# Kernel tuning notes

Measured on AMD Instinct MI355X. Metric: run time of the kernel, lower is better.

The kernel has to match this reference:

```python
import jax, jax.numpy as jnp
import numpy as np

NUM_HEADS = 16
LN_EPS = 1e-05


def setup_inputs() -> dict:
    key = jax.random.key(0)
    ks = jax.random.split(key, 10)
    B, S, H = 2, 2048, 1024
    s = 1.0 / np.sqrt(H)
    return {
        "hidden_states": jax.random.normal(ks[0], (B, S, H), dtype=jnp.float32),
        "Wq": jax.random.normal(ks[1], (H, H), dtype=jnp.float32) * s,
        "bq": jax.random.normal(ks[2], (H,), dtype=jnp.float32) * 0.02,
        "Wk": jax.random.normal(ks[3], (H, H), dtype=jnp.float32) * s,
        "bk": jax.random.normal(ks[4], (H,), dtype=jnp.float32) * 0.02,
        "Wv": jax.random.normal(ks[5], (H, H), dtype=jnp.float32) * s,
        "bv": jax.random.normal(ks[6], (H,), dtype=jnp.float32) * 0.02,
        "Wd": jax.random.normal(ks[7], (H, H), dtype=jnp.float32) * s,
        "bd": jax.random.normal(ks[8], (H,), dtype=jnp.float32) * 0.02,
        "ln_gamma": jnp.ones((H,), dtype=jnp.float32),
        "ln_beta": jnp.zeros((H,), dtype=jnp.float32),
    }


def reference(hidden_states, Wq, bq, Wk, bk, Wv, bv, Wd, bd, ln_gamma, ln_beta):
    B, S, H = hidden_states.shape
    nh = NUM_HEADS
    hd = H // nh

    # QKV projections (torch Linear: x @ W.T + b), split heads -> [B, nh, S, hd]
    def proj(W, b):
        y = jnp.einsum('bsh,oh->bso', hidden_states, W) + b
        return y.reshape(B, S, nh, hd).transpose(0, 2, 1, 3)

    q = proj(Wq, bq)
    k = proj(Wk, bk)
    v = proj(Wv, bv)

    # scaled dot-product attention: [B, nh, S, S]
    scores = jnp.einsum('bhqd,bhkd->bhqk', q, k) / jnp.sqrt(jnp.float32(hd))
    probs = jax.nn.softmax(scores, axis=-1)
    ctx = jnp.einsum('bhqk,bhkd->bhqd', probs, v)  # [B, nh, S, hd]
    ctx = ctx.transpose(0, 2, 1, 3).reshape(B, S, H)

    # output dense + residual + LayerNorm
    attn_out = jnp.einsum('bsh,oh->bso', ctx, Wd) + bd
    x = attn_out + hidden_states
    mu = jnp.mean(x, axis=-1, keepdims=True)
    var = jnp.mean(jnp.square(x - mu), axis=-1, keepdims=True)
    return (x - mu) * jax.lax.rsqrt(var + LN_EPS) * ln_gamma + ln_beta
```

## Files before the change

kernel.cpp:

```cpp
#include <hip/hip_runtime.h>

constexpr int kH    = 1024;
constexpr int kSEQ  = 2048;
constexpr int kBATCH= 2;
constexpr int kNH   = 16;
constexpr int kHD   = 64;
constexpr int kM    = 4096;

typedef _Float16 h8  __attribute__((ext_vector_type(8)));
typedef _Float16 h4  __attribute__((ext_vector_type(4)));
typedef float   f32x4 __attribute__((ext_vector_type(4)));

static __device__ __forceinline__ f32x4 mfma16(h8 a, h8 b, f32x4 c) {
  return __builtin_amdgcn_mfma_f32_16x16x32_f16(a, b, c, 0, 0, 0);
}

static __device__ __forceinline__ void gll16(const _Float16* g, _Float16* l) {
  __builtin_amdgcn_global_load_lds(
      (const __attribute__((address_space(1))) void*)g,
      (__attribute__((address_space(3))) void*)l, 16, 0, 0);
}

#define QSCALE 0.18033688011112042f
#define C0INIT (-5.770780163555854f)

__global__ __launch_bounds__(256) void cvt_all(
    const float* __restrict__ X,  const float* __restrict__ Wq,
    const float* __restrict__ Wk, const float* __restrict__ Wv,
    const float* __restrict__ Wd,
    _Float16* __restrict__ Xh,  _Float16* __restrict__ Wqh,
    _Float16* __restrict__ Wkh, _Float16* __restrict__ Wvh,
    _Float16* __restrict__ Wdh)
{
  int i = blockIdx.x * 256 + threadIdx.x;
  const float* src; _Float16* dst; int off;
  if (i < (kM * kH) / 4) {
    src = X; dst = Xh; off = i;
  } else {
    int j = i - (kM * kH) / 4;
    int w = j >> 18;
    off = j & 262143;
    src = (w == 0) ? Wq : (w == 1) ? Wk : (w == 2) ? Wv : Wd;
    dst = (w == 0) ? Wqh : (w == 1) ? Wkh : (w == 2) ? Wvh : Wdh;
  }
  float4 v = reinterpret_cast<const float4*>(src)[off];
  h4 o;
  o[0] = (_Float16)v.x; o[1] = (_Float16)v.y;
  o[2] = (_Float16)v.z; o[3] = (_Float16)v.w;
  reinterpret_cast<h4*>(dst)[off] = o;
}

__global__ __launch_bounds__(256, 2) void qkv_gemm(
    const _Float16* __restrict__ Xh,
    const _Float16* __restrict__ Wq, const _Float16* __restrict__ Wk,
    const _Float16* __restrict__ Wv,
    const float* __restrict__ bq, const float* __restrict__ bk,
    const float* __restrict__ bv,
    _Float16* __restrict__ Qo, _Float16* __restrict__ Ko, _Float16* __restrict__ Vo)
{
  const int proj = blockIdx.z;
  const _Float16* W   = (proj == 0) ? Wq : ((proj == 1) ? Wk : Wv);
  const float*    bias= (proj == 0) ? bq : ((proj == 1) ? bk : bv);
  _Float16*       Out = (proj == 0) ? Qo : ((proj == 1) ? Ko : Vo);

  const int m0 = blockIdx.y * 128, n0 = blockIdx.x * 128;
  __shared__ __align__(16) _Float16 As[2][128 * 32];
  __shared__ __align__(16) _Float16 Bs[2][128 * 32];

  const int tid  = threadIdx.x;
  const int wave = tid >> 6, lane = tid & 63, quad = lane >> 4, l16 = lane & 15;
  const int mw = (wave & 1) * 64, nw = (wave >> 1) * 64;

  f32x4 acc[4][4] = {};
  const int grow = wave * 32 + (lane >> 2);
  const int gcol = (lane & 3) * 8;
  const _Float16* Ag = Xh + (size_t)(m0 + grow) * kH + gcol;
  const _Float16* Bg = W  + (size_t)(n0 + grow) * kH + gcol;

  {
    gll16(Ag,            &As[0][wave * 1024]);
    gll16(Ag + 16 * kH,  &As[0][wave * 1024 + 512]);
    gll16(Bg,            &Bs[0][wave * 1024]);
    gll16(Bg + 16 * kH,  &Bs[0][wave * 1024 + 512]);
  }

  for (int k = 0; k < 32; ++k) {
    const int cur = k & 1;
    __syncthreads();
    if (k < 31) {
      const int k0 = (k + 1) * 32, nb = cur ^ 1;
      gll16(Ag + k0,           &As[nb][wave * 1024]);
      gll16(Ag + 16 * kH + k0, &As[nb][wave * 1024 + 512]);
      gll16(Bg + k0,           &Bs[nb][wave * 1024]);
      gll16(Bg + 16 * kH + k0, &Bs[nb][wave * 1024 + 512]);
    }
    h8 af[4], bf[4];
    #pragma unroll
    for (int mi = 0; mi < 4; ++mi)
      af[mi] = *reinterpret_cast<const h8*>(&As[cur][(mw + mi * 16 + l16) * 32 + quad * 8]);
    #pragma unroll
    for (int ni = 0; ni < 4; ++ni)
      bf[ni] = *reinterpret_cast<const h8*>(&Bs[cur][(nw + ni * 16 + l16) * 32 + quad * 8]);
    #pragma unroll
    for (int mi = 0; mi < 4; ++mi)
      #pragma unroll
      for (int ni = 0; ni < 4; ++ni)
        acc[mi][ni] = mfma16(af[mi], bf[ni], acc[mi][ni]);
  }

  #pragma unroll
  for (int mi = 0; mi < 4; ++mi)
  #pragma unroll
  for (int ni = 0; ni < 4; ++ni) {
    const int ng = n0 + nw + ni * 16 + l16;
    const float bv_ = bias[ng];
    const int hh = ng >> 6, dd = ng & 63;
    #pragma unroll
    for (int r = 0; r < 4; ++r) {
      const int mg = m0 + mw + mi * 16 + quad * 4 + r;
      float val = acc[mi][ni][r] + bv_;
      if (proj == 0) val *= QSCALE;
      const int bb = mg >> 11, srow = mg & 2047;
      Out[(((size_t)(bb * kNH + hh) * kSEQ) + srow) * kHD + dd] = (_Float16)val;
    }
  }
}

__global__ __launch_bounds__(256) void vtrans(const _Float16* __restrict__ V,
                                              _Float16* __restrict__ Vt)
{
  const int st = blockIdx.x;
  const int bh = blockIdx.y;
  __shared__ __align__(16) _Float16 Lt[64][72];
  const int t = threadIdx.x, r = t >> 2, c = (t & 3) * 16;
  const _Float16* src = V + (size_t)bh * kSEQ * kHD + (size_t)(st * 64 + r) * kHD + c;
  h8 p0 = *reinterpret_cast<const h8*>(src);
  h8 p1 = *reinterpret_cast<const h8*>(src + 8);
  #pragma unroll
  for (int e = 0; e < 8; ++e) Lt[c + e][r] = p0[e];
  #pragma unroll
  for (int e = 0; e < 8; ++e) Lt[c + 8 + e][r] = p1[e];
  __syncthreads();
  _Float16* dst = Vt + (size_t)bh * kHD * kSEQ + (size_t)r * kSEQ + st * 64 + c;
  *reinterpret_cast<h8*>(dst)     = *reinterpret_cast<const h8*>(&Lt[r][c]);
  *reinterpret_cast<h8*>(dst + 8) = *reinterpret_cast<const h8*>(&Lt[r][c + 8]);
}

__global__ __launch_bounds__(256, 3) void attn_kernel(
    const _Float16* __restrict__ Q, const _Float16* __restrict__ K,
    const _Float16* __restrict__ Vt, _Float16* __restrict__ Ctx)
{
  const int qt = blockIdx.x, bh = blockIdx.y;
  const int tid = threadIdx.x;
  const int wave = tid >> 6, lane = tid & 63, quad = lane >> 4, l16 = lane & 15;
  const int sw = l16 & 7;

  __shared__ __align__(16) _Float16 Kl[2][64 * 64];
  __shared__ __align__(16) _Float16 Vl[2][64 * 64];
  __shared__ __align__(16) _Float16 Pl[4][32 * 64];

  const _Float16* Qb = Q  + (size_t)bh * kSEQ * kHD;
  const _Float16* Kb = K  + (size_t)bh * kSEQ * kHD;
  const _Float16* Vb = Vt + (size_t)bh * kHD * kSEQ;

  const int qbase = qt * 128 + wave * 32;
  h8 qf[2][2];
  #pragma unroll
  for (int qh = 0; qh < 2; ++qh)
    #pragma unroll
    for (int dh = 0; dh < 2; ++dh)
      qf[qh][dh] = *reinterpret_cast<const h8*>(
          &Qb[(size_t)(qbase + qh * 16 + l16) * kHD + dh * 32 + quad * 8]);

  const int srow0  = lane >> 3;
  const int schunk = (lane & 7) ^ srow0;
  const int krow   = wave * 16 + srow0;
  const _Float16* Kg = Kb + (size_t)krow * kHD + schunk * 8;
  const _Float16* Vg = Vb + (size_t)krow * kSEQ + schunk * 8;
  _Float16* PlW = Pl[wave];

  float l_acc0 = 0.f, l_acc1 = 0.f;
  f32x4 o[2][4] = {};

  {
    gll16(Kg,                 &Kl[0][(wave * 16) * 64]);
    gll16(Kg + 8 * kHD,       &Kl[0][(wave * 16 + 8) * 64]);
    gll16(Vg,                 &Vl[0][(wave * 16) * 64]);
    gll16(Vg + 8 * kSEQ,      &Vl[0][(wave * 16 + 8) * 64]);
  }

  for (int kt = 0; kt < kSEQ / 64; ++kt) {
    const int cur = kt & 1;
    __syncthreads();
    if (kt + 1 < kSEQ / 64) {
      const int nb = cur ^ 1;
      const size_t ko = (size_t)(kt + 1) * 64;
      gll16(Kg + ko * kHD,             &Kl[nb][(wave * 16) * 64]);
      gll16(Kg + (ko + 8) * kHD,       &Kl[nb][(wave * 16 + 8) * 64]);
      gll16(Vg + ko,                   &Vl[nb][(wave * 16) * 64]);
      gll16(Vg + 8 * kSEQ + ko,        &Vl[nb][(wave * 16 + 8) * 64]);
    }
    const _Float16* Kc = Kl[cur];
    const _Float16* Vc = Vl[cur];

    f32x4 s[4][2];
    #pragma unroll
    for (int nt = 0; nt < 4; ++nt) {
      const int keyl = nt * 16 + l16;
      h8 ka0 = *reinterpret_cast<const h8*>(&Kc[keyl * 64 + ((quad     ) ^ sw) * 8]);
      h8 ka1 = *reinterpret_cast<const h8*>(&Kc[keyl * 64 + ((quad ^ 4) ^ sw) * 8]);
      #pragma unroll
      for (int qh = 0; qh < 2; ++qh) {
        f32x4 a = {C0INIT, C0INIT, C0INIT, C0INIT};
        a = mfma16(ka0, qf[qh][0], a);
        a = mfma16(ka1, qf[qh][1], a);
        s[nt][qh] = a;
      }
    }
    #pragma unroll
    for (int nt = 0; nt < 4; ++nt)
      #pragma unroll
      for (int qh = 0; qh < 2; ++qh) {
        float e0 = exp2f(s[nt][qh][0]);
        float e1 = exp2f(s[nt][qh][1]);
        float e2 = exp2f(s[nt][qh][2]);
        float e3 = exp2f(s[nt][qh][3]);
        float t4 = (e0 + e1) + (e2 + e3);
        if (qh == 0) l_acc0 += t4; else l_acc1 += t4;
        h4 pp;
        pp[0] = (_Float16)e0; pp[1] = (_Float16)e1;
        pp[2] = (_Float16)e2; pp[3] = (_Float16)e3;
        const int c8 = (nt * 2 + (quad >> 1)) ^ sw;
        *reinterpret_cast<h4*>(&PlW[(qh * 16 + l16) * 64 + c8 * 8 + (quad & 1) * 4]) = pp;
      }
    #pragma unroll
    for (int kc = 0; kc < 2; ++kc) {
      const int cs = ((kc * 4 + quad) ^ sw) * 8;
      h8 pa0 = *reinterpret_cast<const h8*>(&PlW[l16 * 64 + cs]);
      h8 pa1 = *reinterpret_cast<const h8*>(&PlW[(16 + l16) * 64 + cs]);
      #pragma unroll
      for (int dt = 0; dt < 4; ++dt) {
        h8 vbf = *reinterpret_cast<const h8*>(&Vc[(dt * 16 + l16) * 64 + cs]);
        o[0][dt] = mfma16(pa0, vbf, o[0][dt]);
        o[1][dt] = mfma16(pa1, vbf, o[1][dt]);
      }
    }
  }

  float li[2] = {l_acc0, l_acc1};
  #pragma unroll
  for (int qh = 0; qh < 2; ++qh) {
    li[qh] += __shfl_xor(li[qh], 16);
    li[qh] += __shfl_xor(li[qh], 32);
    li[qh] = 1.f / li[qh];
  }
  const int b = bh >> 4, hh = bh & 15;
  #pragma unroll
  for (int qh = 0; qh < 2; ++qh)
    #pragma unroll
    for (int r = 0; r < 4; ++r) {
      const float linv = __shfl(li[qh], quad * 4 + r);
      const int srow = qbase + qh * 16 + quad * 4 + r;
      #pragma unroll
      for (int dt = 0; dt < 4; ++dt) {
        const int col = hh * kHD + dt * 16 + l16;
        Ctx[((size_t)(b * kSEQ + srow)) * kH + col] =
            (_Float16)(o[qh][dt][r] * linv);
      }
    }
}

__global__ __launch_bounds__(256, 2) void dense_gemm(
    const _Float16* __restrict__ A, const _Float16* __restrict__ W,
    const float* __restrict__ bias, const float* __restrict__ resid,
    float* __restrict__ Out)
{
  const int m0 = blockIdx.y * 128, n0 = blockIdx.x * 128;
  __shared__ __align__(16) _Float16 As[2][128 * 32];
  __shared__ __align__(16) _Float16 Bs[2][128 * 32];
  const int tid  = threadIdx.x;
  const int wave = tid >> 6, lane = tid & 63, quad = lane >> 4, l16 = lane & 15;
  const int mw = (wave & 1) * 64, nw = (wave >> 1) * 64;
  f32x4 acc[4][4] = {};
  const int grow = wave * 32 + (lane >> 2);
  const int gcol = (lane & 3) * 8;
  const _Float16* Ag = A + (size_t)(m0 + grow) * kH + gcol;
  const _Float16* Bg = W + (size_t)(n0 + grow) * kH + gcol;

  {
    gll16(Ag,           &As[0][wave * 1024]);
    gll16(Ag + 16 * kH, &As[0][wave * 1024 + 512]);
    gll16(Bg,           &Bs[0][wave * 1024]);
    gll16(Bg + 16 * kH, &Bs[0][wave * 1024 + 512]);
  }

  for (int k = 0; k < 32; ++k) {
    const int cur = k & 1;
    __syncthreads();
    if (k < 31) {
      const int k0 = (k + 1) * 32, nb = cur ^ 1;
      gll16(Ag + k0,           &As[nb][wave * 1024]);
      gll16(Ag + 16 * kH + k0, &As[nb][wave * 1024 + 512]);
      gll16(Bg + k0,           &Bs[nb][wave * 1024]);
      gll16(Bg + 16 * kH + k0, &Bs[nb][wave * 1024 + 512]);
    }
    h8 af[4], bf[4];
    #pragma unroll
    for (int mi = 0; mi < 4; ++mi)
      af[mi] = *reinterpret_cast<const h8*>(&As[cur][(mw + mi * 16 + l16) * 32 + quad * 8]);
    #pragma unroll
    for (int ni = 0; ni < 4; ++ni)
      bf[ni] = *reinterpret_cast<const h8*>(&Bs[cur][(nw + ni * 16 + l16) * 32 + quad * 8]);
    #pragma unroll
    for (int mi = 0; mi < 4; ++mi)
      #pragma unroll
      for (int ni = 0; ni < 4; ++ni)
        acc[mi][ni] = mfma16(af[mi], bf[ni], acc[mi][ni]);
  }
  #pragma unroll
  for (int mi = 0; mi < 4; ++mi)
  #pragma unroll
  for (int ni = 0; ni < 4; ++ni) {
    const int ng = n0 + nw + ni * 16 + l16;
    const float bv_ = bias[ng];
    #pragma unroll
    for (int r = 0; r < 4; ++r) {
      const int mg = m0 + mw + mi * 16 + quad * 4 + r;
      Out[(size_t)mg * kH + ng] = acc[mi][ni][r] + bv_ + resid[(size_t)mg * kH + ng];
    }
  }
}

__global__ __launch_bounds__(256) void ln_kernel(const float* __restrict__ Tmp,
    const float* __restrict__ gamma, const float* __restrict__ beta,
    float* __restrict__ out)
{
  const int row = blockIdx.x;
  const float4 v = reinterpret_cast<const float4*>(Tmp + (size_t)row * kH)[threadIdx.x];
  float s  = v.x + v.y + v.z + v.w;
  float ss = v.x * v.x + v.y * v.y + v.z * v.z + v.w * v.w;
  #pragma unroll
  for (int off = 32; off > 0; off >>= 1) {
    s  += __shfl_down(s, off);
    ss += __shfl_down(ss, off);
  }
  __shared__ float red[8];
  const int wave = threadIdx.x >> 6, lane = threadIdx.x & 63;
  if (lane == 0) { red[wave] = s; red[4 + wave] = ss; }
  __syncthreads();
  s  = red[0] + red[1] + red[2] + red[3];
  ss = red[4] + red[5] + red[6] + red[7];
  const float mu   = s * (1.f / kH);
  const float var  = ss * (1.f / kH) - mu * mu;
  const float rstd = rsqrtf(var + 1e-5f);
  const float4 g  = reinterpret_cast<const float4*>(gamma)[threadIdx.x];
  const float4 bb = reinterpret_cast<const float4*>(beta)[threadIdx.x];
  float4 o;
  o.x = (v.x - mu) * rstd * g.x + bb.x;
  o.y = (v.y - mu) * rstd * g.y + bb.y;
  o.z = (v.z - mu) * rstd * g.z + bb.z;
  o.w = (v.w - mu) * rstd * g.w + bb.w;
  reinterpret_cast<float4*>(out + (size_t)row * kH)[threadIdx.x] = o;
}

extern "C" void kernel_launch(void* const* d_in, const int* in_sizes, int n_in,
                              void* d_out, int out_size, void* d_ws, size_t ws_size,
                              hipStream_t stream) {
  const float* hs    = (const float*)d_in[0];
  const float* Wq    = (const float*)d_in[1];
  const float* bq    = (const float*)d_in[2];
  const float* Wk    = (const float*)d_in[3];
  const float* bk    = (const float*)d_in[4];
  const float* Wv    = (const float*)d_in[5];
  const float* bv    = (const float*)d_in[6];
  const float* Wd    = (const float*)d_in[7];
  const float* bd    = (const float*)d_in[8];
  const float* gamma = (const float*)d_in[9];
  const float* beta  = (const float*)d_in[10];
  float* out = (float*)d_out;

  char* ws = (char*)d_ws;
  _Float16* Xh  = (_Float16*)(ws + 0);
  _Float16* Wqh = (_Float16*)(ws + 8388608);
  _Float16* Wkh = (_Float16*)(ws + 10485760);
  _Float16* Wvh = (_Float16*)(ws + 12582912);
  _Float16* Wdh = (_Float16*)(ws + 14680064);
  _Float16* Qh  = (_Float16*)(ws + 16777216);
  _Float16* Kh  = (_Float16*)(ws + 25165824);
  _Float16* Vh  = (_Float16*)(ws + 33554432);
  _Float16* Ch  = (_Float16*)(ws + 41943040);
  _Float16* Vtb = Xh;
  float*    Tmp = (float*)Qh;

  cvt_all<<<8192, 256, 0, stream>>>(hs, Wq, Wk, Wv, Wd, Xh, Wqh, Wkh, Wvh, Wdh);
  qkv_gemm<<<dim3(kH / 128, kM / 128, 3), 256, 0, stream>>>(
      Xh, Wqh, Wkh, Wvh, bq, bk, bv, Qh, Kh, Vh);
  vtrans<<<dim3(kSEQ / 64, kBATCH * kNH), 256, 0, stream>>>(Vh, Vtb);
  attn_kernel<<<dim3(kSEQ / 128, kBATCH * kNH), 256, 0, stream>>>(Qh, Kh, Vtb, Ch);
  dense_gemm<<<dim3(kH / 128, kM / 128), 256, 0, stream>>>(Ch, Wdh, bd, hs, Tmp);
  ln_kernel<<<kM, 256, 0, stream>>>(Tmp, gamma, beta, out);
}
```

Measured before the change: 232.8 us.

## Split attention into 8 waves of 16 queries and halve dense GEMM N-tile

The attention kernel now runs 512 threads per block, with each of 8 waves handling 16 query rows instead of 4 waves handling 32. Each thread issues fewer K/V loads, and MFMA sections are wrapped in s_setprio to favour matrix issue. The dense projection GEMM uses 128x64 tiles, doubling its grid to 512 blocks so more CUs stay busy. The aim is more waves in flight per CU and better CU fill. In exchange, K/V fragments in LDS are reused across fewer query rows per wave, and B-tile reuse per block is lower.

```diff
diff --git a/kernel.cpp b/kernel.cpp
--- a/kernel.cpp
+++ b/kernel.cpp
@@ -146,7 +146,7 @@
   *reinterpret_cast<h8*>(dst + 8) = *reinterpret_cast<const h8*>(&Lt[r][c + 8]);
 }
 
-__global__ __launch_bounds__(256, 3) void attn_kernel(
+__global__ __launch_bounds__(512, 4) void attn_kernel(
     const _Float16* __restrict__ Q, const _Float16* __restrict__ K,
     const _Float16* __restrict__ Vt, _Float16* __restrict__ Ctx)
 {
@@ -157,36 +157,32 @@
 
   __shared__ __align__(16) _Float16 Kl[2][64 * 64];
   __shared__ __align__(16) _Float16 Vl[2][64 * 64];
-  __shared__ __align__(16) _Float16 Pl[4][32 * 64];
+  __shared__ __align__(16) _Float16 Pl[8][16 * 64];
 
   const _Float16* Qb = Q  + (size_t)bh * kSEQ * kHD;
   const _Float16* Kb = K  + (size_t)bh * kSEQ * kHD;
   const _Float16* Vb = Vt + (size_t)bh * kHD * kSEQ;
 
-  const int qbase = qt * 128 + wave * 32;
-  h8 qf[2][2];
-  #pragma unroll
-  for (int qh = 0; qh < 2; ++qh)
-    #pragma unroll
-    for (int dh = 0; dh < 2; ++dh)
-      qf[qh][dh] = *reinterpret_cast<const h8*>(
-          &Qb[(size_t)(qbase + qh * 16 + l16) * kHD + dh * 32 + quad * 8]);
+  const int qbase = qt * 128 + wave * 16;
+  h8 qf[2];
+  #pragma unroll
+  for (int dh = 0; dh < 2; ++dh)
+    qf[dh] = *reinterpret_cast<const h8*>(
+        &Qb[(size_t)(qbase + l16) * kHD + dh * 32 + quad * 8]);
 
   const int srow0  = lane >> 3;
   const int schunk = (lane & 7) ^ srow0;
-  const int krow   = wave * 16 + srow0;
+  const int krow   = wave * 8 + srow0;
   const _Float16* Kg = Kb + (size_t)krow * kHD + schunk * 8;
   const _Float16* Vg = Vb + (size_t)krow * kSEQ + schunk * 8;
   _Float16* PlW = Pl[wave];
 
-  float l_acc0 = 0.f, l_acc1 = 0.f;
-  f32x4 o[2][4] = {};
+  float l_acc = 0.f;
+  f32x4 o[4] = {};
 
   {
-    gll16(Kg,                 &Kl[0][(wave * 16) * 64]);
-    gll16(Kg + 8 * kHD,       &Kl[0][(wave * 16 + 8) * 64]);
-    gll16(Vg,                 &Vl[0][(wave * 16) * 64]);
-    gll16(Vg + 8 * kSEQ,      &Vl[0][(wave * 16 + 8) * 64]);
+    gll16(Kg, &Kl[0][(wave * 8) * 64]);
+    gll16(Vg, &Vl[0][(wave * 8) * 64]);
   }
 
   for (int kt = 0; kt < kSEQ / 64; ++kt) {
@@ -195,79 +191,76 @@
     if (kt + 1 < kSEQ / 64) {
       const int nb = cur ^ 1;
       const size_t ko = (size_t)(kt + 1) * 64;
-      gll16(Kg + ko * kHD,             &Kl[nb][(wave * 16) * 64]);
-      gll16(Kg + (ko + 8) * kHD,       &Kl[nb][(wave * 16 + 8) * 64]);
-      gll16(Vg + ko,                   &Vl[nb][(wave * 16) * 64]);
-      gll16(Vg + 8 * kSEQ + ko,        &Vl[nb][(wave * 16 + 8) * 64]);
+      gll16(Kg + ko * kHD, &Kl[nb][(wave * 8) * 64]);
+      gll16(Vg + ko,       &Vl[nb][(wave * 8) * 64]);
     }
     const _Float16* Kc = Kl[cur];
     const _Float16* Vc = Vl[cur];
 
-    f32x4 s[4][2];
+    h8 ka[4][2];
     #pragma unroll
     for (int nt = 0; nt < 4; ++nt) {
       const int keyl = nt * 16 + l16;
-      h8 ka0 = *reinterpret_cast<const h8*>(&Kc[keyl * 64 + ((quad     ) ^ sw) * 8]);
-      h8 ka1 = *reinterpret_cast<const h8*>(&Kc[keyl * 64 + ((quad ^ 4) ^ sw) * 8]);
-      #pragma unroll
-      for (int qh = 0; qh < 2; ++qh) {
-        f32x4 a = {C0INIT, C0INIT, C0INIT, C0INIT};
-        a = mfma16(ka0, qf[qh][0], a);
-        a = mfma16(ka1, qf[qh][1], a);
-        s[nt][qh] = a;
-      }
-    }
-    #pragma unroll
-    for (int nt = 0; nt < 4; ++nt)
-      #pragma unroll
-      for (int qh = 0; qh < 2; ++qh) {
-        float e0 = exp2f(s[nt][qh][0]);
-        float e1 = exp2f(s[nt][qh][1]);
-        float e2 = exp2f(s[nt][qh][2]);
-        float e3 = exp2f(s[nt][qh][3]);
-        float t4 = (e0 + e1) + (e2 + e3);
-        if (qh == 0) l_acc0 += t4; else l_acc1 += t4;
-        h4 pp;
-        pp[0] = (_Float16)e0; pp[1] = (_Float16)e1;
-        pp[2] = (_Float16)e2; pp[3] = (_Float16)e3;
-        const int c8 = (nt * 2 + (quad >> 1)) ^ sw;
-        *reinterpret_cast<h4*>(&PlW[(qh * 16 + l16) * 64 + c8 * 8 + (quad & 1) * 4]) = pp;
-      }
+      ka[nt][0] = *reinterpret_cast<const h8*>(&Kc[keyl * 64 + ((quad     ) ^ sw) * 8]);
+      ka[nt][1] = *reinterpret_cast<const h8*>(&Kc[keyl * 64 + ((quad ^ 4) ^ sw) * 8]);
+    }
+    f32x4 s[4];
+    __builtin_amdgcn_s_setprio(1);
+    #pragma unroll
+    for (int nt = 0; nt < 4; ++nt) {
+      f32x4 a = {C0INIT, C0INIT, C0INIT, C0INIT};
+      a = mfma16(ka[nt][0], qf[0], a);
+      a = mfma16(ka[nt][1], qf[1], a);
+      s[nt] = a;
+    }
+    __builtin_amdgcn_s_setprio(0);
+
+    #pragma unroll
+    for (int nt = 0; nt < 4; ++nt) {
+      float e0 = exp2f(s[nt][0]);
+      float e1 = exp2f(s[nt][1]);
+      float e2 = exp2f(s[nt][2]);
+      float e3 = exp2f(s[nt][3]);
+      l_acc += (e0 + e1) + (e2 + e3);
+      h4 pp;
+      pp[0] = (_Float16)e0; pp[1] = (_Float16)e1;
+      pp[2] = (_Float16)e2; pp[3] = (_Float16)e3;
+      const int c8 = (nt * 2 + (quad >> 1)) ^ sw;
+      *reinterpret_cast<h4*>(&PlW[l16 * 64 + c8 * 8 + (quad & 1) * 4]) = pp;
+    }
+
     #pragma unroll
     for (int kc = 0; kc < 2; ++kc) {
       const int cs = ((kc * 4 + quad) ^ sw) * 8;
-      h8 pa0 = *reinterpret_cast<const h8*>(&PlW[l16 * 64 + cs]);
-      h8 pa1 = *reinterpret_cast<const h8*>(&PlW[(16 + l16) * 64 + cs]);
-      #pragma unroll
-      for (int dt = 0; dt < 4; ++dt) {
-        h8 vbf = *reinterpret_cast<const h8*>(&Vc[(dt * 16 + l16) * 64 + cs]);
-        o[0][dt] = mfma16(pa0, vbf, o[0][dt]);
-        o[1][dt] = mfma16(pa1, vbf, o[1][dt]);
-      }
-    }
-  }
-
-  float li[2] = {l_acc0, l_acc1};
-  #pragma unroll
-  for (int qh = 0; qh < 2; ++qh) {
-    li[qh] += __shfl_xor(li[qh], 16);
-    li[qh] += __shfl_xor(li[qh], 32);
-    li[qh] = 1.f / li[qh];
-  }
+      h8 pa = *reinterpret_cast<const h8*>(&PlW[l16 * 64 + cs]);
+      h8 vb0 = *reinterpret_cast<const h8*>(&Vc[(0 * 16 + l16) * 64 + cs]);
+      h8 vb1 = *reinterpret_cast<const h8*>(&Vc[(1 * 16 + l16) * 64 + cs]);
+      h8 vb2 = *reinterpret_cast<const h8*>(&Vc[(2 * 16 + l16) * 64 + cs]);
+      h8 vb3 = *reinterpret_cast<const h8*>(&Vc[(3 * 16 + l16) * 64 + cs]);
+      __builtin_amdgcn_s_setprio(1);
+      o[0] = mfma16(pa, vb0, o[0]);
+      o[1] = mfma16(pa, vb1, o[1]);
+      o[2] = mfma16(pa, vb2, o[2]);
+      o[3] = mfma16(pa, vb3, o[3]);
+      __builtin_amdgcn_s_setprio(0);
+    }
+  }
+
+  float li = l_acc;
+  li += __shfl_xor(li, 16);
+  li += __shfl_xor(li, 32);
+  li = 1.f / li;
   const int b = bh >> 4, hh = bh & 15;
   #pragma unroll
-  for (int qh = 0; qh < 2; ++qh)
-    #pragma unroll
-    for (int r = 0; r < 4; ++r) {
-      const float linv = __shfl(li[qh], quad * 4 + r);
-      const int srow = qbase + qh * 16 + quad * 4 + r;
-      #pragma unroll
-      for (int dt = 0; dt < 4; ++dt) {
-        const int col = hh * kHD + dt * 16 + l16;
-        Ctx[((size_t)(b * kSEQ + srow)) * kH + col] =
-            (_Float16)(o[qh][dt][r] * linv);
-      }
-    }
+  for (int r = 0; r < 4; ++r) {
+    const float linv = __shfl(li, quad * 4 + r);
+    const int srow = qbase + quad * 4 + r;
+    #pragma unroll
+    for (int dt = 0; dt < 4; ++dt) {
+      const int col = hh * kHD + dt * 16 + l16;
+      Ctx[((size_t)(b * kSEQ + srow)) * kH + col] = (_Float16)(o[dt][r] * linv);
+    }
+  }
 }
 
 __global__ __launch_bounds__(256, 2) void dense_gemm(
@@ -275,23 +268,23 @@
     const float* __restrict__ bias, const float* __restrict__ resid,
     float* __restrict__ Out)
 {
-  const int m0 = blockIdx.y * 128, n0 = blockIdx.x * 128;
+  const int m0 = blockIdx.y * 128, n0 = blockIdx.x * 64;
   __shared__ __align__(16) _Float16 As[2][128 * 32];
-  __shared__ __align__(16) _Float16 Bs[2][128 * 32];
+  __shared__ __align__(16) _Float16 Bs[2][64 * 32];
   const int tid  = threadIdx.x;
   const int wave = tid >> 6, lane = tid & 63, quad = lane >> 4, l16 = lane & 15;
-  const int mw = (wave & 1) * 64, nw = (wave >> 1) * 64;
-  f32x4 acc[4][4] = {};
-  const int grow = wave * 32 + (lane >> 2);
+  const int mw = (wave & 1) * 64, nw = (wave >> 1) * 32;
+  f32x4 acc[4][2] = {};
+  const int growA = wave * 32 + (lane >> 2);
+  const int growB = wave * 16 + (lane >> 2);
   const int gcol = (lane & 3) * 8;
-  const _Float16* Ag = A + (size_t)(m0 + grow) * kH + gcol;
-  const _Float16* Bg = W + (size_t)(n0 + grow) * kH + gcol;
+  const _Float16* Ag = A + (size_t)(m0 + growA) * kH + gcol;
+  const _Float16* Bg = W + (size_t)(n0 + growB) * kH + gcol;
 
   {
     gll16(Ag,           &As[0][wave * 1024]);
     gll16(Ag + 16 * kH, &As[0][wave * 1024 + 512]);
-    gll16(Bg,           &Bs[0][wave * 1024]);
-    gll16(Bg + 16 * kH, &Bs[0][wave * 1024 + 512]);
+    gll16(Bg,           &Bs[0][wave * 512]);
   }
 
   for (int k = 0; k < 32; ++k) {
@@ -301,26 +294,25 @@
       const int k0 = (k + 1) * 32, nb = cur ^ 1;
       gll16(Ag + k0,           &As[nb][wave * 1024]);
       gll16(Ag + 16 * kH + k0, &As[nb][wave * 1024 + 512]);
-      gll16(Bg + k0,           &Bs[nb][wave * 1024]);
-      gll16(Bg + 16 * kH + k0, &Bs[nb][wave * 1024 + 512]);
-    }
-    h8 af[4], bf[4];
+      gll16(Bg + k0,           &Bs[nb][wave * 512]);
+    }
+    h8 af[4], bf[2];
     #pragma unroll
     for (int mi = 0; mi < 4; ++mi)
       af[mi] = *reinterpret_cast<const h8*>(&As[cur][(mw + mi * 16 + l16) * 32 + quad * 8]);
     #pragma unroll
-    for (int ni = 0; ni < 4; ++ni)
+    for (int ni = 0; ni < 2; ++ni)
       bf[ni] = *reinterpret_cast<const h8*>(&Bs[cur][(nw + ni * 16 + l16) * 32 + quad * 8]);
     #pragma unroll
     for (int mi = 0; mi < 4; ++mi)
       #pragma unroll
-      for (int ni = 0; ni < 4; ++ni)
+      for (int ni = 0; ni < 2; ++ni)
         acc[mi][ni] = mfma16(af[mi], bf[ni], acc[mi][ni]);
   }
   #pragma unroll
   for (int mi = 0; mi < 4; ++mi)
   #pragma unroll
-  for (int ni = 0; ni < 4; ++ni) {
+  for (int ni = 0; ni < 2; ++ni) {
     const int ng = n0 + nw + ni * 16 + l16;
     const float bv_ = bias[ng];
     #pragma unroll
@@ -396,7 +388,7 @@
   qkv_gemm<<<dim3(kH / 128, kM / 128, 3), 256, 0, stream>>>(
       Xh, Wqh, Wkh, Wvh, bq, bk, bv, Qh, Kh, Vh);
   vtrans<<<dim3(kSEQ / 64, kBATCH * kNH), 256, 0, stream>>>(Vh, Vtb);
-  attn_kernel<<<dim3(kSEQ / 128, kBATCH * kNH), 256, 0, stream>>>(Qh, Kh, Vtb, Ch);
-  dense_gemm<<<dim3(kH / 128, kM / 128), 256, 0, stream>>>(Ch, Wdh, bd, hs, Tmp);
+  attn_kernel<<<dim3(kSEQ / 128, kBATCH * kNH), 512, 0, stream>>>(Qh, Kh, Vtb, Ch);
+  dense_gemm<<<dim3(kH / 64, kM / 128), 256, 0, stream>>>(Ch, Wdh, bd, hs, Tmp);
   ln_kernel<<<kM, 256, 0, stream>>>(Tmp, gamma, beta, out);
 }
```

Result: faster. 220.2 us (-5.4%).
